# Kernel tuning notes

Measured on AMD Instinct MI355X. Metric: run time of the kernel, lower is better.

Reference implementation:

```python
import jax, jax.numpy as jnp
import numpy as np

B, S, D = 4, 2048, 1024
E, K, H = 8, 2, 2048  # experts, top_k, swiglu hidden (ff_multiplier=2.0)
EPS = 1e-8
RMS_EPS = 1e-6
ROPE_BASE = 10000.0


def setup_inputs() -> dict:
    key = jax.random.key(0)
    ks = jax.random.split(key, 6)
    scale_in = 1.0 / np.sqrt(D)
    scale_h = 1.0 / np.sqrt(H)
    return {
        "x": jax.random.normal(ks[0], (B, S, D), jnp.float32),
        "norm_w": jnp.ones((D,), jnp.float32),
        "router_W": jax.random.normal(ks[1], (E, D), jnp.float32) * scale_in,  # nn.Linear weight [E,D]
        "w1": jax.random.normal(ks[2], (E, H, D), jnp.float32) * scale_in,  # gate proj per expert
        "w3": jax.random.normal(ks[3], (E, H, D), jnp.float32) * scale_in,  # up proj per expert
        "w2": jax.random.normal(ks[4], (E, D, H), jnp.float32) * scale_h,   # down proj per expert
    }


def _rmsnorm(x, w):
    var = jnp.mean(jnp.square(x), axis=-1, keepdims=True)
    return x * jax.lax.rsqrt(var + RMS_EPS) * w


def _rope(x):
    # half-split rotary embedding over full embed dim; x: [B,S,D]
    d2 = D // 2
    inv_freq = 1.0 / (ROPE_BASE ** (jnp.arange(0, d2, dtype=jnp.float32) / d2))
    ang = jnp.arange(S, dtype=jnp.float32)[:, None] * inv_freq[None, :]  # [S,D/2]
    cos, sin = jnp.cos(ang), jnp.sin(ang)
    x1, x2 = x[..., :d2], x[..., d2:]
    return jnp.concatenate([x1 * cos - x2 * sin, x1 * sin + x2 * cos], axis=-1)


def reference(x, norm_w, router_W, w1, w3, w2):
    hidden = _rope(_rmsnorm(x, norm_w))  # [B,S,D]
    logits = jnp.einsum("bsd,ed->bse", hidden, router_W)
    probs = jax.nn.softmax(logits, axis=-1)
    # sparse top-k renormalized gates
    top_v, top_i = jax.lax.top_k(probs, K)  # [B,S,K]
    sparse = jnp.sum(jax.nn.one_hot(top_i, E, dtype=probs.dtype) * top_v[..., None], axis=-2)  # [B,S,E]
    gates = sparse / jnp.clip(jnp.sum(sparse, axis=-1, keepdims=True), EPS)
    # dense all-expert SwiGLU
    g = jnp.einsum("bsd,ehd->bseh", hidden, w1)
    u = jnp.einsum("bsd,ehd->bseh", hidden, w3)
    act = jax.nn.silu(g) * u
    expert_out = jnp.einsum("bseh,edh->bsed", act, w2)  # [B,S,E,D]
    mixed = jnp.sum(gates[..., None] * expert_out, axis=-2)
    return mixed + x
```

## Files before the change

kernel.cpp:

```cpp
#include <hip/hip_runtime.h>

#define TOKENS 8192
#define Dm 1024
#define Hm 2048
#define Sm 2048
#define D2 512
#define SLOTS 16384
#define PADU 256
#define SLOTPAD (SLOTS + 8*PADU)
#define NWE 16777216

#define OF_TAB 0ull
#define OF_HID (OF_TAB + (size_t)Sm*D2*8)
#define OF_ACT (OF_HID + (size_t)TOKENS*Dm*2)
#define OF_W1B (OF_ACT + (size_t)SLOTPAD*Hm*2)
#define OF_W3B (OF_W1B + (size_t)NWE*2)
#define OF_W2B (OF_W3B + (size_t)NWE*2)
#define OF_T2I (OF_W2B + (size_t)NWE*2)
#define OF_T2G (OF_T2I + (size_t)TOKENS*2*4)
#define OF_T2S (OF_T2G + (size_t)TOKENS*2*4)
#define OF_ST  (OF_T2S + (size_t)TOKENS*2*4)
#define OF_SG  (OF_ST + (size_t)SLOTPAD*4)
#define OF_MT  (OF_SG + (size_t)SLOTPAD*4)
#define OF_SO  (OF_MT + 1024)

#define PREP_TOKEN 8192
#define PREP_CONV  (PREP_TOKEN + 3 * (NWE / (256 * 8)))
#define PREP_INIT  (PREP_CONV + (SLOTPAD + 255) / 256)

typedef __bf16 bf16x8 __attribute__((ext_vector_type(8)));
typedef short  s16x8  __attribute__((ext_vector_type(8)));
typedef float  f32x4  __attribute__((ext_vector_type(4)));

__device__ __forceinline__ unsigned short f2bf(float f) {
    union { float f; unsigned u; } v; v.f = f;
    unsigned r = v.u + 0x7fffu + ((v.u >> 16) & 1u);
    return (unsigned short)(r >> 16);
}

__device__ __forceinline__ float bf2f(unsigned short u) {
    union { unsigned u; float f; } v; v.u = ((unsigned)u) << 16;
    return v.f;
}

__device__ __forceinline__ f32x4 mfma16(s16x8 a, s16x8 b, f32x4 c) {
    return __builtin_amdgcn_mfma_f32_16x16x32_bf16(
        __builtin_bit_cast(bf16x8, a), __builtin_bit_cast(bf16x8, b), c, 0, 0, 0);
}

__device__ __forceinline__ void gld16(const void* g, void* l) {
    __builtin_amdgcn_global_load_lds(
        (const __attribute__((address_space(1))) void*)g,
        (__attribute__((address_space(3))) void*)l, 16, 0, 0);
}

__device__ __forceinline__ int xcd_swz(int bid, int nwg) {
    int cpx = nwg >> 3;
    return (bid & 7) * cpx + (bid >> 3);
}

__global__ void k_table(float2* tab) {
    int i = blockIdx.x * 256 + threadIdx.x;
    int s = i >> 9, j = i & 511;
    float inv = expf(-(float)j * (9.210340371976184f / 512.0f));
    float ang = (float)s * inv;
    tab[i] = make_float2(cosf(ang), sinf(ang));
}

__global__ __launch_bounds__(256) void k_prep(
    const float* __restrict__ x, const float* __restrict__ nw,
    const float* __restrict__ rW, const float2* __restrict__ tab,
    const float* __restrict__ w1, const float* __restrict__ w3,
    const float* __restrict__ w2,
    unsigned short* __restrict__ hid, int* __restrict__ t2i,
    float* __restrict__ t2g,
    unsigned short* __restrict__ d1, unsigned short* __restrict__ d3,
    unsigned short* __restrict__ d2,
    int* __restrict__ slot_token, int* __restrict__ meta)
{
    __shared__ float red[4];
    __shared__ float rl[4][8];
    int bid = blockIdx.x;
    int tid = threadIdx.x;

    if (bid >= PREP_CONV) {
        int i = (bid - PREP_CONV) * 256 + tid;
        if (i < SLOTPAD) slot_token[i] = -1;
        if (i < 8) meta[i] = 0;
        return;
    }
    if (bid >= PREP_TOKEN) {
        size_t i = ((size_t)(bid - PREP_TOKEN) * 256 + tid) * 8;
        const float* s; unsigned short* d;
        if (i < (size_t)NWE)            { s = w1; d = d1; }
        else if (i < 2ull * NWE)        { s = w3; d = d3; i -= (size_t)NWE; }
        else                            { s = w2; d = d2; i -= 2ull * NWE; }
        float4 a = *(const float4*)(s + i);
        float4 b = *(const float4*)(s + i + 4);
        s16x8 v;
        v[0]=(short)f2bf(a.x); v[1]=(short)f2bf(a.y); v[2]=(short)f2bf(a.z); v[3]=(short)f2bf(a.w);
        v[4]=(short)f2bf(b.x); v[5]=(short)f2bf(b.y); v[6]=(short)f2bf(b.z); v[7]=(short)f2bf(b.w);
        *(s16x8*)(d + i) = v;
        return;
    }

    int t = bid;
    int lane = tid & 63, wid = tid >> 6;
    int s = t & (Sm - 1);
    const float* xr = x + (size_t)t * Dm;

    float v0 = xr[tid], v1 = xr[tid + 256], v2 = xr[tid + 512], v3 = xr[tid + 768];
    float ss = v0*v0 + v1*v1 + v2*v2 + v3*v3;
    #pragma unroll
    for (int o = 32; o; o >>= 1) ss += __shfl_down(ss, o);
    if (lane == 0) red[wid] = ss;
    __syncthreads();
    float tot = red[0] + red[1] + red[2] + red[3];
    float rms = rsqrtf(tot * (1.0f / Dm) + 1e-6f);

    float n0 = v0 * rms * nw[tid];
    float n1 = v1 * rms * nw[tid + 256];
    float n2 = v2 * rms * nw[tid + 512];
    float n3 = v3 * rms * nw[tid + 768];

    float2 c0 = tab[s * D2 + tid];
    float2 c1 = tab[s * D2 + tid + 256];
    float h0 = n0 * c0.x - n2 * c0.y;
    float h2 = n0 * c0.y + n2 * c0.x;
    float h1 = n1 * c1.x - n3 * c1.y;
    float h3 = n1 * c1.y + n3 * c1.x;

    size_t base = (size_t)t * Dm;
    hid[base + tid]       = f2bf(h0);
    hid[base + tid + 256] = f2bf(h1);
    hid[base + tid + 512] = f2bf(h2);
    hid[base + tid + 768] = f2bf(h3);

    float p[8];
    #pragma unroll
    for (int e = 0; e < 8; e++) {
        const float* r = rW + (size_t)e * Dm;
        p[e] = h0 * r[tid] + h1 * r[tid + 256] + h2 * r[tid + 512] + h3 * r[tid + 768];
    }
    #pragma unroll
    for (int e = 0; e < 8; e++)
        #pragma unroll
        for (int o = 32; o; o >>= 1) p[e] += __shfl_down(p[e], o);
    if (lane == 0) {
        #pragma unroll
        for (int e = 0; e < 8; e++) rl[wid][e] = p[e];
    }
    __syncthreads();
    if (tid == 0) {
        float lg[8];
        #pragma unroll
        for (int e = 0; e < 8; e++) lg[e] = rl[0][e] + rl[1][e] + rl[2][e] + rl[3][e];
        float m = lg[0];
        #pragma unroll
        for (int e = 1; e < 8; e++) m = fmaxf(m, lg[e]);
        int i0 = 0; float b0 = lg[0];
        #pragma unroll
        for (int e = 1; e < 8; e++) if (lg[e] > b0) { b0 = lg[e]; i0 = e; }
        int i1 = -1; float b1 = -3.0e38f;
        #pragma unroll
        for (int e = 0; e < 8; e++) if (e != i0 && lg[e] > b1) { b1 = lg[e]; i1 = e; }
        float p0 = expf(b0 - m), p1 = expf(b1 - m);
        float inv = 1.0f / (p0 + p1);
        t2i[2 * t] = i0; t2i[2 * t + 1] = i1;
        t2g[2 * t] = p0 * inv; t2g[2 * t + 1] = p1 * inv;
    }
}

__global__ __launch_bounds__(256) void k_hist(const int* __restrict__ t2i,
                                              int* __restrict__ meta) {
    __shared__ int h[8];
    int tid = threadIdx.x;
    if (tid < 8) h[tid] = 0;
    __syncthreads();
    int base = blockIdx.x * 512 + tid * 2;
    atomicAdd(&h[t2i[base]], 1);
    atomicAdd(&h[t2i[base + 1]], 1);
    __syncthreads();
    if (tid < 8) atomicAdd(&meta[tid], h[tid]);
}

__global__ void k_offsets(int* meta) {
    if (threadIdx.x == 0 && blockIdx.x == 0) {
        int acc = 0;
        for (int e = 0; e < 8; e++) {
            meta[8 + e] = acc;
            acc += ((meta[e] + PADU - 1) / PADU) * PADU;
        }
        meta[16] = acc;
        for (int e = 0; e < 8; e++) meta[17 + e] = meta[8 + e];
    }
}

__global__ __launch_bounds__(256) void k_place(
    const int* __restrict__ t2i, const float* __restrict__ t2g,
    int* __restrict__ slot_token, float* __restrict__ slot_gate,
    int* __restrict__ t2s, int* __restrict__ meta)
{
    __shared__ int lcnt[8];
    __shared__ int lbase[8];
    int tid = threadIdx.x;
    if (tid < 8) lcnt[tid] = 0;
    __syncthreads();
    int t = blockIdx.x * 256 + tid;
    int e0 = t2i[2 * t], e1 = t2i[2 * t + 1];
    int r0 = atomicAdd(&lcnt[e0], 1);
    int r1 = atomicAdd(&lcnt[e1], 1);
    __syncthreads();
    if (tid < 8) lbase[tid] = atomicAdd(&meta[17 + tid], lcnt[tid]);
    __syncthreads();
    int p0 = lbase[e0] + r0, p1 = lbase[e1] + r1;
    slot_token[p0] = t; slot_gate[p0] = t2g[2 * t];     t2s[2 * t]     = p0;
    slot_token[p1] = t; slot_gate[p1] = t2g[2 * t + 1]; t2s[2 * t + 1] = p1;
}

__global__ __launch_bounds__(512, 2) void k_gemm1(
    const unsigned short* __restrict__ hid,
    const unsigned short* __restrict__ w1b, const unsigned short* __restrict__ w3b,
    const int* __restrict__ slot_token, unsigned short* __restrict__ act,
    const int* __restrict__ meta)
{
    int nwg = gridDim.x * gridDim.y;
    int bid = blockIdx.y * gridDim.x + blockIdx.x;
    int wg  = xcd_swz(bid, nwg);
    int bx  = wg % gridDim.x, by = wg / gridDim.x;

    int row0 = by * 256;
    if (row0 >= meta[16]) return;
    int e = 0;
    #pragma unroll
    for (int q = 1; q < 8; q++) if (row0 >= meta[8 + q]) e = q;
    int h0 = bx * 128;

    __shared__ unsigned short As[2][256 * 64];
    __shared__ unsigned short Bs[2][256 * 64];

    int tid = threadIdx.x, lane = tid & 63, w = tid >> 6;
    int wm = w >> 2, wn = w & 3;
    int wrow = wm * 128, wcol = wn * 32;
    int frow = lane & 15, q4 = lane >> 4;
    int rx = frow & 7;

    int grow = tid >> 3;
    int sslot = (tid & 7) ^ (grow & 7);

    const unsigned short* srcA[4];
    const unsigned short* srcB[4];
    #pragma unroll
    for (int g = 0; g < 4; g++) {
        int ra = g * 64 + grow;
        int tok = slot_token[row0 + ra];  if (tok < 0) tok = 0;
        srcA[g] = hid + (size_t)tok * Dm + sslot * 8;
        int rb = g * 64 + grow;
        srcB[g] = (rb < 128 ? w1b + ((size_t)e * Hm + h0 + rb) * Dm
                            : w3b + ((size_t)e * Hm + h0 + rb - 128) * Dm) + sslot * 8;
    }

    s16x8 a8[4][2], bG[2][2], bU[2][2];
    f32x4 accG[8][2] = {};
    f32x4 accU[8][2] = {};

#define SA(nb, g) gld16(srcA[g] + koff, (unsigned short*)&As[(nb)][(g) * 4096 + tid * 8])
#define SB(nb, g) gld16(srcB[g] + koff, (unsigned short*)&Bs[(nb)][(g) * 4096 + tid * 8])

#define RD_A(buf, half) do {                                                  \
    _Pragma("unroll") for (int i_ = 0; i_ < 4; i_++)                          \
    _Pragma("unroll") for (int kh_ = 0; kh_ < 2; kh_++) {                     \
        int sp_ = ((kh_ << 2) | q4) ^ rx;                                     \
        a8[i_][kh_] = *(const s16x8*)&As[(buf)][(wrow + (half) * 64 + i_ * 16 + frow) * 64 + sp_ * 8]; \
    } } while (0)

#define RD_B(buf, arr, base) do {                                             \
    _Pragma("unroll") for (int j_ = 0; j_ < 2; j_++)                          \
    _Pragma("unroll") for (int kh_ = 0; kh_ < 2; kh_++) {                     \
        int sp_ = ((kh_ << 2) | q4) ^ rx;                                     \
        arr[j_][kh_] = *(const s16x8*)&Bs[(buf)][((base) + wcol + j_ * 16 + frow) * 64 + sp_ * 8]; \
    } } while (0)

#define MFMA_Q(accX, bX, half) do {                                           \
    _Pragma("unroll") for (int i_ = 0; i_ < 4; i_++)                          \
    _Pragma("unroll") for (int j_ = 0; j_ < 2; j_++)                          \
    _Pragma("unroll") for (int kh_ = 0; kh_ < 2; kh_++)                       \
        accX[(half) * 4 + i_][j_] = mfma16(a8[i_][kh_], bX[j_][kh_], accX[(half) * 4 + i_][j_]); \
    } while (0)

#define COMP1(buf) do {                                                       \
    RD_A(buf, 0);                                                             \
    RD_B(buf, bG, 0);                                                         \
    MFMA_Q(accG, bG, 0);                                                      \
    RD_B(buf, bU, 128);                                                       \
    MFMA_Q(accU, bU, 0);                                                      \
    RD_A(buf, 1);                                                             \
    MFMA_Q(accG, bG, 1);                                                      \
    MFMA_Q(accU, bU, 1);                                                      \
    } while (0)

    {
        int koff = 0;
        #pragma unroll
        for (int g = 0; g < 4; g++) SA(0, g);
        #pragma unroll
        for (int g = 0; g < 4; g++) SB(0, g);
    }

    for (int kt = 0; kt < 15; ++kt) {
        int buf = kt & 1, nbuf = buf ^ 1;
        {
            int koff = (kt + 1) * 64;
            #pragma unroll
            for (int g = 0; g < 4; g++) SA(nbuf, g);
            #pragma unroll
            for (int g = 0; g < 4; g++) SB(nbuf, g);
        }
        asm volatile("s_waitcnt vmcnt(8)" ::: "memory");
        __builtin_amdgcn_s_barrier();
        __builtin_amdgcn_sched_barrier(0);
        COMP1(buf);
        __builtin_amdgcn_sched_barrier(0);
        __builtin_amdgcn_s_barrier();
    }
    asm volatile("s_waitcnt vmcnt(0)" ::: "memory");
    __builtin_amdgcn_s_barrier();
    __builtin_amdgcn_sched_barrier(0);
    COMP1(1);

#undef SA
#undef SB
#undef RD_A
#undef RD_B
#undef MFMA_Q
#undef COMP1

    #pragma unroll
    for (int m = 0; m < 8; m++)
        #pragma unroll
        for (int j = 0; j < 2; j++)
            #pragma unroll
            for (int r = 0; r < 4; r++) {
                int sr = row0 + wrow + m * 16 + q4 * 4 + r;
                int hc = h0 + wcol + j * 16 + frow;
                float g = accG[m][j][r], u = accU[m][j][r];
                float a = g / (1.0f + expf(-g)) * u;
                act[(size_t)sr * Hm + hc] = f2bf(a);
            }
}

__global__ __launch_bounds__(256) void k_gemm2(
    const unsigned short* __restrict__ act, const unsigned short* __restrict__ w2b,
    const float* __restrict__ slot_gate,
    unsigned short* __restrict__ sout, const int* __restrict__ meta)
{
    int nwg = gridDim.x * gridDim.y;
    int bid = blockIdx.y * gridDim.x + blockIdx.x;
    int wg  = xcd_swz(bid, nwg);
    int bx  = wg % gridDim.x, by = wg / gridDim.x;

    int row0 = by * 128;
    if (row0 >= meta[16]) return;
    int e = 0;
    #pragma unroll
    for (int q = 1; q < 8; q++) if (row0 >= meta[8 + q]) e = q;
    int d0 = bx * 128;

    __shared__ unsigned short As[2][128 * 64];
    __shared__ unsigned short Bs[2][128 * 64];
    __shared__ float sgat[128];

    int tid = threadIdx.x, lane = tid & 63, w = tid >> 6;
    int wm = w >> 1, wn = w & 1;
    int frow = lane & 15, q4 = lane >> 4;
    int rx = frow & 7;

    if (tid < 128) sgat[tid] = slot_gate[row0 + tid];

    int r7 = (tid >> 3) & 7;
    int sslot = (tid & 7) ^ r7;

    const unsigned short* srcA[4];
    const unsigned short* srcB[4];
    #pragma unroll
    for (int i = 0; i < 4; i++) {
        int rr = i * 32 + (tid >> 3);
        srcA[i] = act + (size_t)(row0 + rr) * Hm + sslot * 8;
        srcB[i] = w2b + ((size_t)e * Dm + d0 + rr) * Hm + sslot * 8;
    }

    f32x4 acc[4][4] = {};

#define STAGE2(buf, k0) do {                                                  \
    unsigned short* la_ = &As[(buf)][tid * 8];                                \
    unsigned short* lb_ = &Bs[(buf)][tid * 8];                                \
    _Pragma("unroll")                                                         \
    for (int i_ = 0; i_ < 4; i_++) {                                          \
        gld16(srcA[i_] + (k0), la_ + i_ * 2048);                              \
        gld16(srcB[i_] + (k0), lb_ + i_ * 2048);                              \
    } } while (0)

#define COMP2(buf) do {                                                       \
    _Pragma("unroll")                                                         \
    for (int h_ = 0; h_ < 2; h_++) {                                          \
        int sp_ = ((h_ << 2) | q4) ^ rx;                                      \
        s16x8 am_[4], bn_[4];                                                 \
        _Pragma("unroll")                                                     \
        for (int i_ = 0; i_ < 4; i_++)                                        \
            am_[i_] = *(const s16x8*)&As[(buf)][(wm * 64 + i_ * 16 + frow) * 64 + sp_ * 8]; \
        _Pragma("unroll")                                                     \
        for (int j_ = 0; j_ < 4; j_++)                                        \
            bn_[j_] = *(const s16x8*)&Bs[(buf)][(wn * 64 + j_ * 16 + frow) * 64 + sp_ * 8]; \
        _Pragma("unroll")                                                     \
        for (int i_ = 0; i_ < 4; i_++)                                        \
            _Pragma("unroll")                                                 \
            for (int j_ = 0; j_ < 4; j_++)                                    \
                acc[i_][j_] = mfma16(am_[i_], bn_[j_], acc[i_][j_]);          \
    } } while (0)

    STAGE2(0, 0);
    #pragma unroll 2
    for (int kt = 0; kt < 31; ++kt) {
        STAGE2((kt + 1) & 1, (kt + 1) * 64);
        asm volatile("s_waitcnt vmcnt(8)" ::: "memory");
        __builtin_amdgcn_s_barrier();
        __builtin_amdgcn_sched_barrier(0);
        COMP2(kt & 1);
        __builtin_amdgcn_sched_barrier(0);
        __builtin_amdgcn_s_barrier();
    }
    asm volatile("s_waitcnt vmcnt(0)" ::: "memory");
    __builtin_amdgcn_s_barrier();
    __builtin_amdgcn_sched_barrier(0);
    COMP2(1);

#undef STAGE2
#undef COMP2

    #pragma unroll
    for (int i = 0; i < 4; i++) {
        #pragma unroll
        for (int r = 0; r < 4; r++) {
            int srl = wm * 64 + i * 16 + q4 * 4 + r;
            float gate = sgat[srl];
            size_t rb = (size_t)(row0 + srl) * Dm;
            #pragma unroll
            for (int j = 0; j < 4; j++) {
                int dc = d0 + wn * 64 + j * 16 + frow;
                sout[rb + dc] = f2bf(gate * acc[i][j][r]);
            }
        }
    }
}

__global__ __launch_bounds__(256) void k_final(
    const float* __restrict__ x, const unsigned short* __restrict__ sout,
    const int* __restrict__ t2s, float* __restrict__ out)
{
    int t = blockIdx.x;
    int tid = threadIdx.x;
    int s0 = t2s[2 * t], s1 = t2s[2 * t + 1];
    const float4*  xr = (const float4*)(x + (size_t)t * Dm);
    const ushort4* a  = (const ushort4*)(sout + (size_t)s0 * Dm);
    const ushort4* b  = (const ushort4*)(sout + (size_t)s1 * Dm);
    float4* o = (float4*)(out + (size_t)t * Dm);
    float4 xv = xr[tid];
    ushort4 av = a[tid], bv = b[tid];
    float4 r;
    r.x = xv.x + bf2f(av.x) + bf2f(bv.x);
    r.y = xv.y + bf2f(av.y) + bf2f(bv.y);
    r.z = xv.z + bf2f(av.z) + bf2f(bv.z);
    r.w = xv.w + bf2f(av.w) + bf2f(bv.w);
    o[tid] = r;
}

extern "C" void kernel_launch(void* const* d_in, const int* in_sizes, int n_in,
                              void* d_out, int out_size, void* d_ws, size_t ws_size,
                              hipStream_t stream) {
    const float* x  = (const float*)d_in[0];
    const float* nw = (const float*)d_in[1];
    const float* rW = (const float*)d_in[2];
    const float* w1 = (const float*)d_in[3];
    const float* w3 = (const float*)d_in[4];
    const float* w2 = (const float*)d_in[5];
    float* out = (float*)d_out;
    char* ws = (char*)d_ws;

    float2* tab = (float2*)(ws + OF_TAB);
    unsigned short* hid = (unsigned short*)(ws + OF_HID);
    unsigned short* act = (unsigned short*)(ws + OF_ACT);
    unsigned short* w1b = (unsigned short*)(ws + OF_W1B);
    unsigned short* w3b = (unsigned short*)(ws + OF_W3B);
    unsigned short* w2b = (unsigned short*)(ws + OF_W2B);
    int*   t2i  = (int*)(ws + OF_T2I);
    float* t2g  = (float*)(ws + OF_T2G);
    int*   t2s  = (int*)(ws + OF_T2S);
    int*   stok = (int*)(ws + OF_ST);
    float* sgat = (float*)(ws + OF_SG);
    int*   meta = (int*)(ws + OF_MT);
    unsigned short* sout = (unsigned short*)(ws + OF_SO);

    k_table<<<(Sm * D2) / 256, 256, 0, stream>>>(tab);
    k_prep<<<PREP_INIT, 256, 0, stream>>>(x, nw, rW, tab, w1, w3, w2,
                                          hid, t2i, t2g, w1b, w3b, w2b,
                                          stok, meta);
    k_hist<<<32, 256, 0, stream>>>(t2i, meta);
    k_offsets<<<1, 64, 0, stream>>>(meta);
    k_place<<<TOKENS / 256, 256, 0, stream>>>(t2i, t2g, stok, sgat, t2s, meta);

    dim3 g1(Hm / 128, SLOTPAD / 256);
    k_gemm1<<<g1, 512, 0, stream>>>(hid, w1b, w3b, stok, act, meta);
    dim3 g2(Dm / 128, SLOTPAD / 128);
    k_gemm2<<<g2, 256, 0, stream>>>(act, w2b, sgat, sout, meta);
    k_final<<<TOKENS, 256, 0, stream>>>(x, sout, t2s, out);
}
```

Measured before the change: 388.1 us.

## Interleave global loads with MFMA phases and add setprio in gemm1 mainloop

Restructures the k_gemm1 main loop into four phases. Each phase issues LDS reads and a slice of the next tile's global-to-shared loads, then runs an MFMA block at raised wave priority, followed by partial vmcnt waits and barriers. This replaces the bulk prefetch followed by a single compute block, aiming to spread memory traffic across compute and let MFMA-issuing waves win arbitration. It also drops the min-blocks-per-CU launch bound, which frees register allocation but may reduce occupancy. The added barriers and fine-grained waitcnt bookkeeping risk extra stalls or ordering mistakes.

```diff
diff --git a/kernel.cpp b/kernel.cpp
--- a/kernel.cpp
+++ b/kernel.cpp
@@ -218,7 +218,7 @@
     slot_token[p1] = t; slot_gate[p1] = t2g[2 * t + 1]; t2s[2 * t + 1] = p1;
 }
 
-__global__ __launch_bounds__(512, 2) void k_gemm1(
+__global__ __launch_bounds__(512) void k_gemm1(
     const unsigned short* __restrict__ hid,
     const unsigned short* __restrict__ w1b, const unsigned short* __restrict__ w3b,
     const int* __restrict__ slot_token, unsigned short* __restrict__ act,
@@ -288,52 +288,60 @@
         accX[(half) * 4 + i_][j_] = mfma16(a8[i_][kh_], bX[j_][kh_], accX[(half) * 4 + i_][j_]); \
     } while (0)
 
-#define COMP1(buf) do {                                                       \
-    RD_A(buf, 0);                                                             \
-    RD_B(buf, bG, 0);                                                         \
-    MFMA_Q(accG, bG, 0);                                                      \
-    RD_B(buf, bU, 128);                                                       \
-    MFMA_Q(accU, bU, 0);                                                      \
-    RD_A(buf, 1);                                                             \
-    MFMA_Q(accG, bG, 1);                                                      \
-    MFMA_Q(accU, bU, 1);                                                      \
-    } while (0)
+#define PH_PRE  do { __builtin_amdgcn_s_barrier();                            \
+    asm volatile("s_waitcnt lgkmcnt(0)" ::: "memory");                        \
+    __builtin_amdgcn_sched_barrier(0);                                        \
+    __builtin_amdgcn_s_setprio(1); } while (0)
+#define PH_CLOSE(N) do { __builtin_amdgcn_s_setprio(0);                       \
+    asm volatile("s_waitcnt vmcnt(" #N ")" ::: "memory");                     \
+    __builtin_amdgcn_s_barrier(); } while (0)
+#define PH_CLOSE_NW do { __builtin_amdgcn_s_setprio(0);                       \
+    __builtin_amdgcn_s_barrier(); } while (0)
 
     {
         int koff = 0;
-        #pragma unroll
-        for (int g = 0; g < 4; g++) SA(0, g);
-        #pragma unroll
-        for (int g = 0; g < 4; g++) SB(0, g);
-    }
+        SA(0, 0); SA(0, 2); SB(0, 0); SB(0, 1);
+        SB(0, 2); SB(0, 3); SA(0, 1); SA(0, 3);
+    }
+    asm volatile("s_waitcnt vmcnt(4)" ::: "memory");
+    __builtin_amdgcn_s_barrier();
 
     for (int kt = 0; kt < 15; ++kt) {
         int buf = kt & 1, nbuf = buf ^ 1;
-        {
-            int koff = (kt + 1) * 64;
-            #pragma unroll
-            for (int g = 0; g < 4; g++) SA(nbuf, g);
-            #pragma unroll
-            for (int g = 0; g < 4; g++) SB(nbuf, g);
-        }
-        asm volatile("s_waitcnt vmcnt(8)" ::: "memory");
-        __builtin_amdgcn_s_barrier();
+        int koff = (kt + 1) * 64;
+        RD_A(buf, 0); RD_B(buf, bG, 0);
+        SA(nbuf, 0); SA(nbuf, 2); SB(nbuf, 0); SB(nbuf, 1);
+        PH_PRE; MFMA_Q(accG, bG, 0); PH_CLOSE(6);
+        RD_B(buf, bU, 128);
+        SB(nbuf, 2); SB(nbuf, 3);
+        PH_PRE; MFMA_Q(accU, bU, 0); PH_CLOSE(6);
+        RD_A(buf, 1);
+        SA(nbuf, 1); SA(nbuf, 3);
+        PH_PRE; MFMA_Q(accG, bG, 1); PH_CLOSE_NW;
+        __builtin_amdgcn_s_setprio(1);
+        MFMA_Q(accU, bU, 1);
+        PH_CLOSE(4);
         __builtin_amdgcn_sched_barrier(0);
-        COMP1(buf);
-        __builtin_amdgcn_sched_barrier(0);
-        __builtin_amdgcn_s_barrier();
-    }
-    asm volatile("s_waitcnt vmcnt(0)" ::: "memory");
-    __builtin_amdgcn_s_barrier();
-    __builtin_amdgcn_sched_barrier(0);
-    COMP1(1);
+    }
+
+    RD_A(1, 0); RD_B(1, bG, 0);
+    PH_PRE; MFMA_Q(accG, bG, 0); PH_CLOSE(2);
+    RD_B(1, bU, 128);
+    PH_PRE; MFMA_Q(accU, bU, 0); PH_CLOSE(0);
+    RD_A(1, 1);
+    PH_PRE; MFMA_Q(accG, bG, 1); PH_CLOSE_NW;
+    __builtin_amdgcn_s_setprio(1);
+    MFMA_Q(accU, bU, 1);
+    __builtin_amdgcn_s_setprio(0);
 
 #undef SA
 #undef SB
 #undef RD_A
 #undef RD_B
 #undef MFMA_Q
-#undef COMP1
+#undef PH_PRE
+#undef PH_CLOSE
+#undef PH_CLOSE_NW
 
     #pragma unroll
     for (int m = 0; m < 8; m++)
```

Result: faster. 369.7 us (-4.7%).
